# Kernel tuning notes

Hardware: AMD Instinct MI355X
Metric: run time of the kernel (lower is better)

Reference implementation:

```python
import jax, jax.numpy as jnp
import numpy as np

HEADS = 8
DIM_HEAD = 64
SCALE = DIM_HEAD ** -0.5


def setup_inputs() -> dict:
    key = jax.random.key(0)
    ks = jax.random.split(key, 5)
    dim, hidden = 512, HEADS * DIM_HEAD
    b, l = 4, 2048
    return {
        "x": jax.random.normal(ks[0], (b, dim, l), jnp.float32),
        "w_qkv": jax.random.normal(ks[1], (3 * hidden, dim), jnp.float32) * 0.02,
        "b_qkv": jax.random.normal(ks[2], (3 * hidden,), jnp.float32) * 0.02,
        "w_out": jax.random.normal(ks[3], (dim, hidden), jnp.float32) * 0.02,
        "b_out": jax.random.normal(ks[4], (dim,), jnp.float32) * 0.02,
    }


def reference(x, w_qkv, b_qkv, w_out, b_out):
    b, c, l = x.shape
    # Conv1d kernel-size-1 == per-position linear: (b, 3*hidden, l)
    qkv = jnp.einsum('oc,bcl->bol', w_qkv, x) + b_qkv[None, :, None]
    q, k, v = jnp.split(qkv, 3, axis=1)
    # rearrange 'b (h d) l -> b h d l'
    def split_heads(t):
        return t.reshape(b, HEADS, DIM_HEAD, l)
    q, k, v = split_heads(q) * SCALE, split_heads(k), split_heads(v)
    sim = jnp.einsum('bhdi,bhdj->bhij', q, k)  # [b,h,l,l]
    sim = sim - jax.lax.stop_gradient(jnp.max(sim, axis=-1, keepdims=True))
    attn = jax.nn.softmax(sim, axis=-1)
    out = jnp.einsum('bhij,bhdj->bhid', attn, v)  # [b,h,l,d]
    # 'b h l d -> b (h d) l'
    out = out.transpose(0, 1, 3, 2).reshape(b, HEADS * DIM_HEAD, l)
    out = jnp.einsum('oc,bcl->bol', w_out, out) + b_out[None, :, None]
    return out
```

## Files before the change

### kernel.cpp

```cpp
#include <hip/hip_runtime.h>
#include <hip/hip_bf16.h>

#define B 4
#define DIM 512
#define HID 512
#define NH 8
#define DH 64
#define L 2048
#define SCALE 0.125f

typedef __attribute__((ext_vector_type(8))) short bf16x8;
typedef __attribute__((ext_vector_type(4))) float f32x4;

static __device__ __forceinline__ short f32_to_bf16s(float f) {
    __hip_bfloat16 h = __float2bfloat16(f);
    return *reinterpret_cast<short*>(&h);
}
static __device__ __forceinline__ float bf16s_to_f32(short s) {
    return __uint_as_float(((unsigned)(unsigned short)s) << 16);
}

static __device__ __forceinline__ void gl_lds16(const short* g, short* l) {
    __builtin_amdgcn_global_load_lds(
        (const __attribute__((address_space(1))) void*)g,
        (__attribute__((address_space(3))) void*)l, 16, 0, 0);
}

static __device__ __forceinline__ bf16x8 lds_frag(const short* t, int row, int c) {
    bf16x8 v;
    __builtin_memcpy(&v, t + row * 64 + ((c ^ (row & 7)) * 8), 16);
    return v;
}

__global__ __launch_bounds__(256) void prep_w(
    const float* __restrict__ wq, const float* __restrict__ wo,
    short* __restrict__ dst)
{
    const int g = blockIdx.x * 256 + threadIdx.x;
    const int i = g * 4;
    float4 v;
    if (i < 786432) v = *(const float4*)(wq + i);
    else            v = *(const float4*)(wo + (i - 786432));
    short4 pk = {f32_to_bf16s(v.x), f32_to_bf16s(v.y),
                 f32_to_bf16s(v.z), f32_to_bf16s(v.w)};
    *(short4*)(dst + i) = pk;
}

__global__ __launch_bounds__(256) void transpose_x(
    const float* __restrict__ X, short* __restrict__ XT)
{
    const int l0 = blockIdx.x * 64;
    const int c0 = blockIdx.y * 64;
    const int b  = blockIdx.z;
    const int tid = threadIdx.x;

    __shared__ float tile[64][65];
    const float* Xb = X + (size_t)b * DIM * L;

    #pragma unroll
    for (int it = 0; it < 16; ++it) {
        const int cr = (tid >> 6) + it * 4;
        const int lc = tid & 63;
        tile[cr][lc] = Xb[(size_t)(c0 + cr) * L + l0 + lc];
    }
    __syncthreads();
    short* XTb = XT + (size_t)b * L * DIM;
    #pragma unroll
    for (int it = 0; it < 8; ++it) {
        const int l  = (tid >> 5) + it * 8;
        const int c2 = (tid & 31) * 2;
        short2 pk = {f32_to_bf16s(tile[c2][l]), f32_to_bf16s(tile[c2 + 1][l])};
        *(short2*)(XTb + (size_t)(l0 + l) * DIM + c0 + c2) = pk;
    }
}

__global__ __launch_bounds__(256) void qkv_mfma(
    const short* __restrict__ Wb, const short* __restrict__ XT,
    const float* __restrict__ bias,
    short* __restrict__ qws, short* __restrict__ kws, short* __restrict__ vws)
{
    const int lBase = blockIdx.x * 128;
    const int oBase = blockIdx.y * 128;
    const int b     = blockIdx.z;
    const int tid   = threadIdx.x;
    const int wave  = tid >> 6;
    const int lane  = tid & 63;
    const int lid   = lane & 15;
    const int quad  = lane >> 4;
    const int rsub  = lane >> 3;
    const int cl    = (lane & 7) ^ rsub;

    __shared__ __align__(16) short Wt[128 * 64];
    __shared__ __align__(16) short Xt[128 * 64];

    const short* XTb = XT + (size_t)b * L * DIM;
    const int oLoc = (wave & 1) * 64;
    const int lLoc = (wave >> 1) * 64;

    f32x4 acc[4][4];
    #pragma unroll
    for (int mi = 0; mi < 4; ++mi)
        #pragma unroll
        for (int ni = 0; ni < 4; ++ni) acc[mi][ni] = (f32x4){0.f, 0.f, 0.f, 0.f};

    for (int c0 = 0; c0 < DIM; c0 += 64) {
        if (c0) __syncthreads();
        #pragma unroll
        for (int t = 0; t < 4; ++t) {
            const int ch = wave * 4 + t;
            const int r  = ch * 8 + rsub;
            gl_lds16(Wb  + (size_t)(oBase + r) * DIM + c0 + cl * 8, Wt + ch * 512);
            gl_lds16(XTb + (size_t)(lBase + r) * DIM + c0 + cl * 8, Xt + ch * 512);
        }
        __syncthreads();
        #pragma unroll
        for (int kc = 0; kc < 2; ++kc) {
            bf16x8 a[4], bb[4];
            #pragma unroll
            for (int mi = 0; mi < 4; ++mi)
                a[mi] = lds_frag(Wt, oLoc + mi * 16 + lid, kc * 4 + quad);
            #pragma unroll
            for (int ni = 0; ni < 4; ++ni)
                bb[ni] = lds_frag(Xt, lLoc + ni * 16 + lid, kc * 4 + quad);
            #pragma unroll
            for (int mi = 0; mi < 4; ++mi)
                #pragma unroll
                for (int ni = 0; ni < 4; ++ni)
                    acc[mi][ni] = __builtin_amdgcn_mfma_f32_16x16x32_bf16(
                        a[mi], bb[ni], acc[mi][ni], 0, 0, 0);
        }
    }

    const int rty = oBase >> 9;
    const float sc = (rty == 0) ? SCALE : 1.0f;
    const int h = ((oBase + oLoc) >> 6) & 7;

    #pragma unroll
    for (int mi = 0; mi < 4; ++mi) {
        const int dB = mi * 16 + quad * 4;
        float bia[4];
        #pragma unroll
        for (int r = 0; r < 4; ++r)
            bia[r] = bias[oBase + oLoc + mi * 16 + quad * 4 + r];

        if (rty < 2) {
            short* dst = (rty == 0 ? qws : kws) + (((size_t)b * NH + h) * L) * DH;
            #pragma unroll
            for (int ni = 0; ni < 4; ++ni) {
                const int l = lBase + lLoc + ni * 16 + lid;
                short4 pk = {f32_to_bf16s((acc[mi][ni][0] + bia[0]) * sc),
                             f32_to_bf16s((acc[mi][ni][1] + bia[1]) * sc),
                             f32_to_bf16s((acc[mi][ni][2] + bia[2]) * sc),
                             f32_to_bf16s((acc[mi][ni][3] + bia[3]) * sc)};
                *(short4*)(dst + (size_t)l * DH + dB) = pk;
            }
        } else {
            short* dst = vws + (((size_t)b * NH + h) * DH) * L;
            #pragma unroll
            for (int r = 0; r < 4; ++r) {
                const int d = dB + r;
                #pragma unroll
                for (int ni = 0; ni < 4; ++ni)
                    dst[(size_t)d * L + lBase + lLoc + ni * 16 + lid] =
                        f32_to_bf16s((acc[mi][ni][r] + bia[r]) * sc);
            }
        }
    }
}

__global__ __launch_bounds__(256) void attn_mfma(
    const short* __restrict__ Q, const short* __restrict__ K,
    const short* __restrict__ VT,
    float* __restrict__ Op0, float* __restrict__ Op1,
    float* __restrict__ Lp0, float* __restrict__ Lp1)
{
    const int iTile = blockIdx.x;
    const int h     = blockIdx.y;
    const int b     = blockIdx.z >> 1;
    const int half  = blockIdx.z & 1;
    const int tid   = threadIdx.x;
    const int wave  = tid >> 6;
    const int lane  = tid & 63;
    const int lid   = lane & 15;
    const int quad  = lane >> 4;
    const int rsub  = lane >> 3;
    const int cl    = (lane & 7) ^ rsub;

    float* __restrict__ Op = half ? Op1 : Op0;
    float* __restrict__ Lp = half ? Lp1 : Lp0;

    const size_t headOff = ((size_t)b * NH + h) * (size_t)L * DH;
    const short* Qh = Q + headOff;
    const short* Kh = K + headOff;
    const short* Vh = VT + headOff;

    __shared__ __align__(16) short Kt[64 * 64];
    __shared__ __align__(16) short Vt[64 * 64];
    __shared__ __align__(16) short Ps[4 * 16 * 72];
    short* Pw = Ps + wave * 16 * 72;

    const int qrow = iTile * 64 + wave * 16 + lid;
    bf16x8 qf[2];
    qf[0] = *(const bf16x8*)(Qh + (size_t)qrow * DH + quad * 8);
    qf[1] = *(const bf16x8*)(Qh + (size_t)qrow * DH + 32 + quad * 8);

    f32x4 oacc[4];
    #pragma unroll
    for (int nt = 0; nt < 4; ++nt) oacc[nt] = (f32x4){0.f, 0.f, 0.f, 0.f};
    float lsum[4] = {0.f, 0.f, 0.f, 0.f};

    const int jt0 = half * 16;
    for (int jt = jt0; jt < jt0 + 16; ++jt) {
        const int j0 = jt * 64;
        if (jt > jt0) __syncthreads();
        #pragma unroll
        for (int t = 0; t < 2; ++t) {
            const int ch = wave * 2 + t;
            const int r  = ch * 8 + rsub;
            gl_lds16(Kh + (size_t)(j0 + r) * DH + cl * 8, Kt + ch * 512);
            gl_lds16(Vh + (size_t)r * L + j0 + cl * 8,    Vt + ch * 512);
        }
        __syncthreads();

        f32x4 s[4];
        #pragma unroll
        for (int nt = 0; nt < 4; ++nt) {
            bf16x8 kf0 = lds_frag(Kt, nt * 16 + lid, quad);
            bf16x8 kf1 = lds_frag(Kt, nt * 16 + lid, 4 + quad);
            f32x4 z = {0.f, 0.f, 0.f, 0.f};
            z = __builtin_amdgcn_mfma_f32_16x16x32_bf16(qf[0], kf0, z, 0, 0, 0);
            z = __builtin_amdgcn_mfma_f32_16x16x32_bf16(qf[1], kf1, z, 0, 0, 0);
            s[nt] = z;
        }

        #pragma unroll
        for (int nt = 0; nt < 4; ++nt) {
            #pragma unroll
            for (int r = 0; r < 4; ++r) {
                float p = __expf(s[nt][r]);
                short pb = f32_to_bf16s(p);
                Pw[(quad * 4 + r) * 72 + nt * 16 + lid] = pb;
                lsum[r] += bf16s_to_f32(pb);
            }
        }
        __builtin_amdgcn_wave_barrier();

        #pragma unroll
        for (int kc = 0; kc < 2; ++kc) {
            bf16x8 pf;
            __builtin_memcpy(&pf, Pw + lid * 72 + kc * 32 + quad * 8, 16);
            #pragma unroll
            for (int nt = 0; nt < 4; ++nt) {
                bf16x8 vf = lds_frag(Vt, nt * 16 + lid, kc * 4 + quad);
                oacc[nt] = __builtin_amdgcn_mfma_f32_16x16x32_bf16(pf, vf, oacc[nt], 0, 0, 0);
            }
        }
        __builtin_amdgcn_wave_barrier();
    }

    #pragma unroll
    for (int r = 0; r < 4; ++r) {
        float v = lsum[r];
        v += __shfl_xor(v, 1);
        v += __shfl_xor(v, 2);
        v += __shfl_xor(v, 4);
        v += __shfl_xor(v, 8);
        lsum[r] = v;
    }
    const int lg = iTile * 64 + wave * 16 + quad * 4;
    if (lid == 0) {
        float4 ls = {lsum[0], lsum[1], lsum[2], lsum[3]};
        *(float4*)(Lp + ((size_t)b * NH + h) * L + lg) = ls;
    }

    #pragma unroll
    for (int nt = 0; nt < 4; ++nt) {
        const int d = nt * 16 + lid;
        #pragma unroll
        for (int r = 0; r < 4; ++r)
            Op[((size_t)b * L + lg + r) * HID + h * DH + d] = oacc[nt][r];
    }
}

__global__ __launch_bounds__(256) void combine(
    const float* __restrict__ Op0, const float* __restrict__ Op1,
    const float* __restrict__ Lp0, const float* __restrict__ Lp1,
    short* __restrict__ Abf)
{
    const int g = blockIdx.x * 256 + threadIdx.x;
    const int i = g * 4;
    const int b = i >> 20;
    const int rem = i & 1048575;
    const int l = rem >> 9;
    const int c = rem & 511;
    const int h = c >> 6;
    const size_t li = ((size_t)b * NH + h) * L + l;
    const float inv = 1.0f / (Lp0[li] + Lp1[li]);
    const float4 o0 = *(const float4*)(Op0 + i);
    const float4 o1 = *(const float4*)(Op1 + i);
    short4 pk = {f32_to_bf16s((o0.x + o1.x) * inv),
                 f32_to_bf16s((o0.y + o1.y) * inv),
                 f32_to_bf16s((o0.z + o1.z) * inv),
                 f32_to_bf16s((o0.w + o1.w) * inv)};
    *(short4*)(Abf + i) = pk;
}

__global__ __launch_bounds__(256) void out_mfma(
    const short* __restrict__ Wo, const short* __restrict__ Abf,
    const float* __restrict__ bias, float* __restrict__ out)
{
    const int lBase = blockIdx.x * 128;
    const int oBase = blockIdx.y * 64;
    const int b     = blockIdx.z;
    const int tid   = threadIdx.x;
    const int wave  = tid >> 6;
    const int lane  = tid & 63;
    const int lid   = lane & 15;
    const int quad  = lane >> 4;
    const int rsub  = lane >> 3;
    const int cl    = (lane & 7) ^ rsub;

    __shared__ __align__(16) short Wt[64 * 64];
    __shared__ __align__(16) short At[128 * 64];

    const short* Ab = Abf + (size_t)b * L * HID;
    const int oLoc = (wave & 1) * 32;
    const int lLoc = (wave >> 1) * 64;

    f32x4 acc[2][4];
    #pragma unroll
    for (int mi = 0; mi < 2; ++mi)
        #pragma unroll
        for (int ni = 0; ni < 4; ++ni) acc[mi][ni] = (f32x4){0.f, 0.f, 0.f, 0.f};

    for (int c0 = 0; c0 < HID; c0 += 64) {
        if (c0) __syncthreads();
        #pragma unroll
        for (int t = 0; t < 2; ++t) {
            const int ch = wave * 2 + t;
            const int r  = ch * 8 + rsub;
            gl_lds16(Wo + (size_t)(oBase + r) * HID + c0 + cl * 8, Wt + ch * 512);
        }
        #pragma unroll
        for (int t = 0; t < 4; ++t) {
            const int ch = wave * 4 + t;
            const int r  = ch * 8 + rsub;
            gl_lds16(Ab + (size_t)(lBase + r) * HID + c0 + cl * 8, At + ch * 512);
        }
        __syncthreads();
        #pragma unroll
        for (int kc = 0; kc < 2; ++kc) {
            bf16x8 a[2], bb[4];
            #pragma unroll
            for (int mi = 0; mi < 2; ++mi)
                a[mi] = lds_frag(Wt, oLoc + mi * 16 + lid, kc * 4 + quad);
            #pragma unroll
            for (int ni = 0; ni < 4; ++ni)
                bb[ni] = lds_frag(At, lLoc + ni * 16 + lid, kc * 4 + quad);
            #pragma unroll
            for (int mi = 0; mi < 2; ++mi)
                #pragma unroll
                for (int ni = 0; ni < 4; ++ni)
                    acc[mi][ni] = __builtin_amdgcn_mfma_f32_16x16x32_bf16(
                        a[mi], bb[ni], acc[mi][ni], 0, 0, 0);
        }
    }

    #pragma unroll
    for (int mi = 0; mi < 2; ++mi) {
        #pragma unroll
        for (int r = 0; r < 4; ++r) {
            const int o = oBase + oLoc + mi * 16 + quad * 4 + r;
            const float bia = bias[o];
            #pragma unroll
            for (int ni = 0; ni < 4; ++ni)
                out[((size_t)b * DIM + o) * L + lBase + lLoc + ni * 16 + lid] =
                    acc[mi][ni][r] + bia;
        }
    }
}

extern "C" void kernel_launch(void* const* d_in, const int* in_sizes, int n_in,
                              void* d_out, int out_size, void* d_ws, size_t ws_size,
                              hipStream_t stream)
{
    const float* x     = (const float*)d_in[0];
    const float* w_qkv = (const float*)d_in[1];
    const float* b_qkv = (const float*)d_in[2];
    const float* w_out = (const float*)d_in[3];
    const float* b_out = (const float*)d_in[4];
    float* out = (float*)d_out;

    char* w = (char*)d_ws;
    short* xT  = (short*)(w);
    short* wqb = (short*)(w + (8u << 20));
    short* wob = wqb + 786432;
    short* qws = (short*)(w + (10u << 20));
    short* kws = (short*)(w + (18u << 20));
    short* vws = (short*)(w + (26u << 20));
    short* Abf = (short*)(w + (34u << 20));
    float* Op1 = (float*)(w + (42u << 20));
    float* Lp0 = (float*)(w + (58u << 20));
    float* Lp1 = Lp0 + (size_t)B * NH * L;
    float* Op0 = out;

    dim3 blk(256);
    prep_w<<<dim3(1024), blk, 0, stream>>>(w_qkv, w_out, wqb);
    transpose_x<<<dim3(L / 64, DIM / 64, B), blk, 0, stream>>>(x, xT);
    qkv_mfma<<<dim3(L / 128, 1536 / 128, B), blk, 0, stream>>>(
        wqb, xT, b_qkv, qws, kws, vws);
    attn_mfma<<<dim3(L / 64, NH, B * 2), blk, 0, stream>>>(
        qws, kws, vws, Op0, Op1, Lp0, Lp1);
    combine<<<dim3(4096), blk, 0, stream>>>(Op0, Op1, Lp0, Lp1, Abf);
    out_mfma<<<dim3(L / 128, DIM / 64, B), blk, 0, stream>>>(
        wob, Abf, b_out, out);
}
```

Measured before the change: 179.7 us.

## Switch attention to 32x32x16 MFMA with register-resident P via lane shuffles

Rewrites the attention inner loop to use 32x32x16 bf16 MFMAs, with each wave handling 32 query rows and each block 128 query rows. It computes S transposed (K as the A operand, Q as B), so the exp'd probabilities can be repacked into B-operand fragments with cross-half lane shuffles instead of a round trip through LDS. The goal is to drop the P scratch buffer, the wave barriers and LDS traffic, and to raise MFMA efficiency and K/V tile reuse per block. In exchange it halves the grid size and raises register pressure, and the output is now stored as float4 rows.

```diff
diff --git a/kernel.cpp b/kernel.cpp
--- a/kernel.cpp
+++ b/kernel.cpp
@@ -9,8 +9,10 @@
 #define L 2048
 #define SCALE 0.125f
 
-typedef __attribute__((ext_vector_type(8))) short bf16x8;
-typedef __attribute__((ext_vector_type(4))) float f32x4;
+typedef __attribute__((ext_vector_type(8)))  short bf16x8;
+typedef __attribute__((ext_vector_type(4)))  float f32x4;
+typedef __attribute__((ext_vector_type(16))) float f32x16;
+typedef __attribute__((ext_vector_type(4)))  int   i32x4;
 
 static __device__ __forceinline__ short f32_to_bf16s(float f) {
     __hip_bfloat16 h = __float2bfloat16(f);
@@ -181,8 +183,8 @@
     const int tid   = threadIdx.x;
     const int wave  = tid >> 6;
     const int lane  = tid & 63;
-    const int lid   = lane & 15;
-    const int quad  = lane >> 4;
+    const int l5    = lane & 31;
+    const int me    = lane >> 5;
     const int rsub  = lane >> 3;
     const int cl    = (lane & 7) ^ rsub;
 
@@ -196,18 +198,19 @@
 
     __shared__ __align__(16) short Kt[64 * 64];
     __shared__ __align__(16) short Vt[64 * 64];
-    __shared__ __align__(16) short Ps[4 * 16 * 72];
-    short* Pw = Ps + wave * 16 * 72;
-
-    const int qrow = iTile * 64 + wave * 16 + lid;
-    bf16x8 qf[2];
-    qf[0] = *(const bf16x8*)(Qh + (size_t)qrow * DH + quad * 8);
-    qf[1] = *(const bf16x8*)(Qh + (size_t)qrow * DH + 32 + quad * 8);
-
-    f32x4 oacc[4];
-    #pragma unroll
-    for (int nt = 0; nt < 4; ++nt) oacc[nt] = (f32x4){0.f, 0.f, 0.f, 0.f};
-    float lsum[4] = {0.f, 0.f, 0.f, 0.f};
+
+    const int q0 = iTile * 128 + wave * 32;
+    bf16x8 qf[4];
+    #pragma unroll
+    for (int kc = 0; kc < 4; ++kc)
+        qf[kc] = *(const bf16x8*)(Qh + (size_t)(q0 + l5) * DH + kc * 16 + me * 8);
+
+    f32x16 oacc[2];
+    #pragma unroll
+    for (int dt = 0; dt < 2; ++dt)
+        #pragma unroll
+        for (int r = 0; r < 16; ++r) oacc[dt][r] = 0.f;
+    float lsum = 0.f;
 
     const int jt0 = half * 16;
     for (int jt = jt0; jt < jt0 + 16; ++jt) {
@@ -222,63 +225,74 @@
         }
         __syncthreads();
 
-        f32x4 s[4];
-        #pragma unroll
-        for (int nt = 0; nt < 4; ++nt) {
-            bf16x8 kf0 = lds_frag(Kt, nt * 16 + lid, quad);
-            bf16x8 kf1 = lds_frag(Kt, nt * 16 + lid, 4 + quad);
-            f32x4 z = {0.f, 0.f, 0.f, 0.f};
-            z = __builtin_amdgcn_mfma_f32_16x16x32_bf16(qf[0], kf0, z, 0, 0, 0);
-            z = __builtin_amdgcn_mfma_f32_16x16x32_bf16(qf[1], kf1, z, 0, 0, 0);
-            s[nt] = z;
-        }
-
-        #pragma unroll
-        for (int nt = 0; nt < 4; ++nt) {
-            #pragma unroll
-            for (int r = 0; r < 4; ++r) {
-                float p = __expf(s[nt][r]);
-                short pb = f32_to_bf16s(p);
-                Pw[(quad * 4 + r) * 72 + nt * 16 + lid] = pb;
-                lsum[r] += bf16s_to_f32(pb);
-            }
-        }
-        __builtin_amdgcn_wave_barrier();
-
-        #pragma unroll
-        for (int kc = 0; kc < 2; ++kc) {
-            bf16x8 pf;
-            __builtin_memcpy(&pf, Pw + lid * 72 + kc * 32 + quad * 8, 16);
-            #pragma unroll
-            for (int nt = 0; nt < 4; ++nt) {
-                bf16x8 vf = lds_frag(Vt, nt * 16 + lid, kc * 4 + quad);
-                oacc[nt] = __builtin_amdgcn_mfma_f32_16x16x32_bf16(pf, vf, oacc[nt], 0, 0, 0);
-            }
-        }
-        __builtin_amdgcn_wave_barrier();
-    }
-
-    #pragma unroll
-    for (int r = 0; r < 4; ++r) {
-        float v = lsum[r];
-        v += __shfl_xor(v, 1);
-        v += __shfl_xor(v, 2);
-        v += __shfl_xor(v, 4);
-        v += __shfl_xor(v, 8);
-        lsum[r] = v;
-    }
-    const int lg = iTile * 64 + wave * 16 + quad * 4;
-    if (lid == 0) {
-        float4 ls = {lsum[0], lsum[1], lsum[2], lsum[3]};
-        *(float4*)(Lp + ((size_t)b * NH + h) * L + lg) = ls;
-    }
-
-    #pragma unroll
-    for (int nt = 0; nt < 4; ++nt) {
-        const int d = nt * 16 + lid;
-        #pragma unroll
-        for (int r = 0; r < 4; ++r)
-            Op[((size_t)b * L + lg + r) * HID + h * DH + d] = oacc[nt][r];
+        bf16x8 pf[4];
+        #pragma unroll
+        for (int mt = 0; mt < 2; ++mt) {
+            f32x16 s;
+            #pragma unroll
+            for (int r = 0; r < 16; ++r) s[r] = 0.f;
+            #pragma unroll
+            for (int kc = 0; kc < 4; ++kc) {
+                bf16x8 a = lds_frag(Kt, mt * 32 + l5, kc * 2 + me);
+                s = __builtin_amdgcn_mfma_f32_32x32x16_bf16(a, qf[kc], s, 0, 0, 0);
+            }
+            unsigned short pbs[16];
+            #pragma unroll
+            for (int r = 0; r < 16; ++r) {
+                float p = __expf(s[r]);
+                unsigned short pb = (unsigned short)f32_to_bf16s(p);
+                pbs[r] = pb;
+                lsum += bf16s_to_f32((short)pb);
+            }
+            unsigned dw[4][2];
+            #pragma unroll
+            for (int g = 0; g < 4; ++g) {
+                dw[g][0] = (unsigned)pbs[4 * g] | ((unsigned)pbs[4 * g + 1] << 16);
+                dw[g][1] = (unsigned)pbs[4 * g + 2] | ((unsigned)pbs[4 * g + 3] << 16);
+            }
+            #pragma unroll
+            for (int kl = 0; kl < 2; ++kl) {
+                const unsigned own0 = me ? dw[2 * kl + 1][0] : dw[2 * kl][0];
+                const unsigned own1 = me ? dw[2 * kl + 1][1] : dw[2 * kl][1];
+                const unsigned snd0 = me ? dw[2 * kl][0] : dw[2 * kl + 1][0];
+                const unsigned snd1 = me ? dw[2 * kl][1] : dw[2 * kl + 1][1];
+                const unsigned rcv0 = (unsigned)__shfl_xor((int)snd0, 32);
+                const unsigned rcv1 = (unsigned)__shfl_xor((int)snd1, 32);
+                i32x4 bi;
+                bi[0] = (int)(me ? rcv0 : own0);
+                bi[1] = (int)(me ? rcv1 : own1);
+                bi[2] = (int)(me ? own0 : rcv0);
+                bi[3] = (int)(me ? own1 : rcv1);
+                pf[mt * 2 + kl] = __builtin_bit_cast(bf16x8, bi);
+            }
+        }
+
+        #pragma unroll
+        for (int kc = 0; kc < 4; ++kc) {
+            #pragma unroll
+            for (int dt = 0; dt < 2; ++dt) {
+                bf16x8 a = lds_frag(Vt, dt * 32 + l5, kc * 2 + me);
+                oacc[dt] = __builtin_amdgcn_mfma_f32_32x32x16_bf16(a, pf[kc], oacc[dt], 0, 0, 0);
+            }
+        }
+    }
+
+    {
+        float v = lsum + __shfl_xor(lsum, 32);
+        if (me == 0)
+            Lp[((size_t)b * NH + h) * L + q0 + l5] = v;
+    }
+
+    const int qg = q0 + l5;
+    #pragma unroll
+    for (int dt = 0; dt < 2; ++dt) {
+        #pragma unroll
+        for (int g = 0; g < 4; ++g) {
+            const int d = dt * 32 + 8 * g + 4 * me;
+            float4 v = {oacc[dt][4 * g], oacc[dt][4 * g + 1],
+                        oacc[dt][4 * g + 2], oacc[dt][4 * g + 3]};
+            *(float4*)(Op + ((size_t)b * L + qg) * HID + h * DH + d) = v;
+        }
     }
 }
 
@@ -409,7 +423,7 @@
     transpose_x<<<dim3(L / 64, DIM / 64, B), blk, 0, stream>>>(x, xT);
     qkv_mfma<<<dim3(L / 128, 1536 / 128, B), blk, 0, stream>>>(
         wqb, xT, b_qkv, qws, kws, vws);
-    attn_mfma<<<dim3(L / 64, NH, B * 2), blk, 0, stream>>>(
+    attn_mfma<<<dim3(L / 128, NH, B * 2), blk, 0, stream>>>(
         qws, kws, vws, Op0, Op1, Lp0, Lp1);
     combine<<<dim3(4096), blk, 0, stream>>>(Op0, Op1, Lp0, Lp1, Abf);
     out_mfma<<<dim3(L / 128, DIM / 64, B), blk, 0, stream>>>(
```

New measurement: 176.1 us. 1.02x faster.
